# Performance work log

Hardware: AMD Instinct MI355X
Metric: run time of the kernel (lower is better)

The kernel has to match this reference:

```python
import jax, jax.numpy as jnp
import numpy as np

IMG_B, IMG_H, IMG_W, IMG_C = 16, 512, 1024, 3

def _base_grid(B, H, W):
    # replicates the module's custom normalization: arange/dim * 2 - 1
    base_x = (jnp.arange(W, dtype=jnp.float32) / W) * 2.0 - 1.0   # [W]
    base_y = (jnp.arange(H, dtype=jnp.float32) / H) * 2.0 - 1.0   # [H]
    base = jnp.stack([jnp.broadcast_to(base_x[None, :], (H, W)),
                      jnp.broadcast_to(base_y[:, None], (H, W))], axis=-1)  # [H,W,2]
    return jnp.broadcast_to(base[None], (B, H, W, 2))

def _grid_sample_bilinear_zeros(im, grid):
    # im: [B,C,H,W], grid: [B,Ho,Wo,2] in [-1,1], align_corners=False, zeros padding
    B, C, H, W = im.shape
    gx, gy = grid[..., 0], grid[..., 1]
    ix = ((gx + 1.0) * W - 1.0) * 0.5
    iy = ((gy + 1.0) * H - 1.0) * 0.5
    x0 = jnp.floor(ix); y0 = jnp.floor(iy)
    wx1 = ix - x0; wx0 = 1.0 - wx1
    wy1 = iy - y0; wy0 = 1.0 - wy1
    x0i = x0.astype(jnp.int32); y0i = y0.astype(jnp.int32)
    b_idx = jnp.arange(B, dtype=jnp.int32)[:, None, None]

    def corner(xi, yi, w):
        valid = (xi >= 0) & (xi < W) & (yi >= 0) & (yi < H)
        xc = jnp.clip(xi, 0, W - 1); yc = jnp.clip(yi, 0, H - 1)
        # advanced indexing -> [B,Ho,Wo,C]
        v = im[b_idx, :, yc, xc]
        return v * (w * valid.astype(im.dtype))[..., None]

    out = (corner(x0i,     y0i,     wx0 * wy0) +
           corner(x0i + 1, y0i,     wx1 * wy0) +
           corner(x0i,     y0i + 1, wx0 * wy1) +
           corner(x0i + 1, y0i + 1, wx1 * wy1))           # [B,Ho,Wo,C]
    return jnp.transpose(out, (0, 3, 1, 2))                # [B,C,Ho,Wo]

def setup_inputs() -> dict:
    key = jax.random.key(0)
    k1, k2, k3 = jax.random.split(key, 3)
    pred_flow = jax.random.normal(k1, (IMG_B, IMG_H, IMG_W, 2), dtype=jnp.float32) * 8.0
    im1_origin = jax.random.uniform(k2, (IMG_B, IMG_C, IMG_H, IMG_W), dtype=jnp.float32)
    im2_origin = jax.random.uniform(k3, (IMG_B, IMG_C, IMG_H, IMG_W), dtype=jnp.float32)
    return {"pred_flow": pred_flow, "im1_origin": im1_origin, "im2_origin": im2_origin}

def reference(pred_flow, im1_origin, im2_origin):
    B, H, W, _ = pred_flow.shape
    scale = jnp.array([W, H], dtype=pred_flow.dtype)
    grid = pred_flow / scale + _base_grid(B, H, W)
    im1_warp = _grid_sample_bilinear_zeros(im1_origin, grid)
    loss = jnp.sum(jnp.abs(im2_origin - im1_warp)) / (W * H)
    return loss
```

## Files before the change

### kernel.cpp

```cpp
#include <hip/hip_runtime.h>
#include <hip/hip_fp16.h>

namespace {

constexpr int B = 16, C = 3, H = 512, W = 1024;
constexpr int HW = H * W;
constexpr int SLABW = 256, SLABH = 64;
constexpr int XH  = 16;
constexpr int SWD = SLABW + 2 * XH;
constexpr int PAIRS = SWD / 2;
constexpr int PADP = 147;
constexpr int RING = 32;
constexpr int RA = 11;
constexpr int RB = 16;
constexpr int RPS = 4;
constexpr int BLOCK = 1024;
constexpr int TX = W / SLABW;
constexpr int TY = H / SLABH;
constexpr int GRID = B * TX * TY;
constexpr int PF_ROWS = RA + RB + 1;
constexpr int STG_P = C * RPS * PAIRS;
constexpr int CHS = RING * PADP;

constexpr float INV_W = 1.0f / 1024.0f;
constexpr float INV_H = 1.0f / 512.0f;

__device__ __forceinline__ float2 ld2g(const float* p) {
    struct __attribute__((packed, aligned(4))) F2 { float a, b; };
    const F2 v = *reinterpret_cast<const F2*>(p);
    return make_float2(v.a, v.b);
}

__device__ __forceinline__ uint32_t packh2(float a, float b) {
    return (uint32_t)__half_as_ushort(__float2half_rn(a))
         | ((uint32_t)__half_as_ushort(__float2half_rn(b)) << 16);
}
__device__ __forceinline__ float2 unpackh2(uint32_t u) {
    const __half2 h = __builtin_bit_cast(__half2, u);
    return make_float2(__low2float(h), __high2float(h));
}
__device__ __forceinline__ uint32_t alignsel(uint32_t hi, uint32_t lo, int sh) {
    return (uint32_t)(((((uint64_t)hi) << 32) | (uint64_t)lo) >> sh);
}

__global__ __launch_bounds__(BLOCK, 8) void flow_loss_partial(
    const float* __restrict__ flow,
    const float* __restrict__ im1,
    const float* __restrict__ im2,
    float* __restrict__ partials)
{
    __shared__ uint32_t sm32[C * CHS];
    __shared__ float red[BLOCK / 64];

    const int tid = threadIdx.x;
    const int bid = blockIdx.x;
    const int b   = bid >> 5;
    const int tt  = bid & 31;
    const int tyi = tt >> 2;
    const int txi = tt & 3;
    const int xbase  = txi * SLABW;
    const int yStart = tyi * SLABH;
    const int xb0    = xbase - XH;

    const float* __restrict__ im1b = im1 + b * C * HW;
    const float* __restrict__ im2b = im2 + b * C * HW;
    const float* __restrict__ flb  = flow + 2 * (b * HW);

    for (int e = tid; e < PF_ROWS * C * PAIRS; e += BLOCK) {
        const int q  = e % PAIRS;
        const int rc = e / PAIRS;
        const int c  = rc / PF_ROWS;
        const int ri = rc - c * PF_ROWS;
        const int row = yStart - RA + ri;
        if (row >= 0) {
            const int g0 = min(max(xb0 + 2 * q, 0), W - 1);
            const int g1 = min(max(xb0 + 2 * q + 1, 0), W - 1);
            const float a = im1b[c * HW + row * W + g0];
            const float d = im1b[c * HW + row * W + g1];
            sm32[c * CHS + (row & (RING - 1)) * PADP + q] = packh2(a, d);
        }
    }

    int  stSr[2], stG0[2], stG1[2], stL[2];
    const bool stOK1 = (tid < STG_P - BLOCK);
#pragma unroll
    for (int k = 0; k < 2; ++k) {
        const int e  = (k == 0) ? tid : (stOK1 ? BLOCK + tid : 0);
        const int q  = e % PAIRS;
        const int rc = e / PAIRS;
        const int c  = rc >> 2;
        stSr[k] = rc & 3;
        const int g0 = min(max(xb0 + 2 * q, 0), W - 1);
        const int g1 = min(max(xb0 + 2 * q + 1, 0), W - 1);
        stG0[k] = c * HW + g0;
        stG1[k] = c * HW + g1;
        stL[k]  = c * CHS + q;
    }

    auto issue = [&](int r0, int (&sIdx)[2], uint32_t (&sVal)[2]) {
#pragma unroll
        for (int k = 0; k < 2; ++k) {
            const int srow = r0 + stSr[k];
            int idx = -1; uint32_t v = 0;
            const bool act = (k == 0 || stOK1) & (srow < H);
            if (act) {
                const float a = im1b[stG0[k] + (srow << 10)];
                const float d = im1b[stG1[k] + (srow << 10)];
                v   = packh2(a, d);
                idx = stL[k] + (srow & (RING - 1)) * PADP;
            }
            sIdx[k] = idx; sVal[k] = v;
        }
    };

    int sIA[2]; uint32_t sVA[2];
    issue(yStart + RB + 1, sIA, sVA);

    const int colp = tid & (SLABW - 1);
    const int prow = tid >> 8;
    const int x = xbase + colp;
    const float base_x = (float)x * (2.0f * INV_W) - 1.0f;

    __syncthreads();

    float acc = 0.0f;

#pragma unroll 1
    for (int ys = yStart; ys < yStart + SLABH; ys += RPS) {
        int sIB[2]; uint32_t sVB[2];
        issue(ys + RB + 1 + RPS, sIB, sVB);

        const int y = ys + prow;
        const int zoff = y * W + x;
        const float2 f = *reinterpret_cast<const float2*>(flb + 2 * zoff);
        const float z0 = im2b[zoff];
        const float z1 = im2b[HW + zoff];
        const float z2 = im2b[2 * HW + zoff];

        const float base_y = (float)y * (2.0f * INV_H) - 1.0f;
        const float gx = __builtin_fmaf(f.x, INV_W, base_x);
        const float gy = __builtin_fmaf(f.y, INV_H, base_y);
        const float ixf = __builtin_fmaf(gx + 1.0f, 512.0f, -0.5f);
        const float iyf = __builtin_fmaf(gy + 1.0f, 256.0f, -0.5f);

        const float x0f = floorf(ixf), y0f = floorf(iyf);
        const float wx1 = ixf - x0f, wx0 = 1.0f - wx1;
        const float wy1 = iyf - y0f, wy0 = 1.0f - wy1;
        const int x0 = (int)x0f, y0 = (int)y0f;
        const int y1 = y0 + 1;
        const bool vx0 = (x0 >= 0) & (x0 < W);
        const bool vx1 = (x0 >= -1) & (x0 < W - 1);
        const bool vy0 = (y0 >= 0) & (y0 < H);
        const bool vy1 = (y1 >= 0) & (y1 < H);
        const bool s0 = (x0 >= W - 1), s1 = (x0 >= 0);

        const float px0 = wx0 * (float)vx0;
        const float px1 = wx1 * (float)vx1;
        const float u0 = (s0 ? 0.0f : px0) + (s1 ? 0.0f : px1);
        const float u1 = (s0 ? px0 : 0.0f) + (s1 ? px1 : 0.0f);
        const float mT = wy0 * (float)vy0;
        const float mB = wy1 * (float)vy1;
        const float aT0 = mT * u0, aT1 = mT * u1;
        const float aB0 = mB * u0, aB1 = mB * u1;

        const int xL  = min(max(x0, 0), W - 2);
        const int y0c = min(max(y0, 0), H - 1);
        const int y1c = min(max(y1, 0), H - 1);

        const int jj = xL - xbase + XH;
        const bool inR = (y0c >= ys - RA) & (y1c <= ys + RB) &
                         ((unsigned)jj <= (unsigned)(SWD - 2));

        float wp0, wp1, wp2;
        __builtin_amdgcn_s_setprio(1);
        if (inR) {
            const int q  = jj >> 1;
            const int sh = (jj & 1) << 4;
            const int aT = (y0c & (RING - 1)) * PADP + q;
            const int aB = (y1c & (RING - 1)) * PADP + q;
            const uint32_t dT0a = sm32[aT],           dT0b = sm32[aT + 1];
            const uint32_t dB0a = sm32[aB],           dB0b = sm32[aB + 1];
            const uint32_t dT1a = sm32[aT + CHS],     dT1b = sm32[aT + CHS + 1];
            const uint32_t dB1a = sm32[aB + CHS],     dB1b = sm32[aB + CHS + 1];
            const uint32_t dT2a = sm32[aT + 2 * CHS], dT2b = sm32[aT + 2 * CHS + 1];
            const uint32_t dB2a = sm32[aB + 2 * CHS], dB2b = sm32[aB + 2 * CHS + 1];
            const float2 t0 = unpackh2(alignsel(dT0b, dT0a, sh));
            const float2 b0 = unpackh2(alignsel(dB0b, dB0a, sh));
            const float2 t1 = unpackh2(alignsel(dT1b, dT1a, sh));
            const float2 b1 = unpackh2(alignsel(dB1b, dB1a, sh));
            const float2 t2 = unpackh2(alignsel(dT2b, dT2a, sh));
            const float2 b2 = unpackh2(alignsel(dB2b, dB2a, sh));
            wp0 = ((aT0 * t0.x + aT1 * t0.y) + aB0 * b0.x) + aB1 * b0.y;
            wp1 = ((aT0 * t1.x + aT1 * t1.y) + aB0 * b1.x) + aB1 * b1.y;
            wp2 = ((aT0 * t2.x + aT1 * t2.y) + aB0 * b2.x) + aB1 * b2.y;
        } else {
            const int oT = y0c * W + xL, oB = y1c * W + xL;
            const float2 ta = ld2g(im1b + oT),            ba = ld2g(im1b + oB);
            const float2 tb = ld2g(im1b + HW + oT),       bb = ld2g(im1b + HW + oB);
            const float2 tc = ld2g(im1b + 2 * HW + oT),   bc = ld2g(im1b + 2 * HW + oB);
            wp0 = ((aT0 * ta.x + aT1 * ta.y) + aB0 * ba.x) + aB1 * ba.y;
            wp1 = ((aT0 * tb.x + aT1 * tb.y) + aB0 * bb.x) + aB1 * bb.y;
            wp2 = ((aT0 * tc.x + aT1 * tc.y) + aB0 * bc.x) + aB1 * bc.y;
        }
        acc += fabsf(z0 - wp0) + fabsf(z1 - wp1) + fabsf(z2 - wp2);
        __builtin_amdgcn_s_setprio(0);

#pragma unroll
        for (int k = 0; k < 2; ++k)
            if (sIA[k] >= 0) sm32[sIA[k]] = sVA[k];
        __syncthreads();

#pragma unroll
        for (int k = 0; k < 2; ++k) { sIA[k] = sIB[k]; sVA[k] = sVB[k]; }
    }

#pragma unroll
    for (int o = 32; o > 0; o >>= 1)
        acc += __shfl_down(acc, o, 64);
    const int lane = tid & 63;
    const int wid  = tid >> 6;
    if (lane == 0) red[wid] = acc;
    __syncthreads();
    if (tid == 0) {
        float s = 0.0f;
#pragma unroll
        for (int wv = 0; wv < BLOCK / 64; ++wv) s += red[wv];
        partials[bid] = s;
    }
}

__global__ __launch_bounds__(256) void flow_loss_reduce(
    const float* __restrict__ partials, float* __restrict__ out)
{
    __shared__ double lds[256];
    double acc = 0.0;
    for (int i = threadIdx.x; i < GRID; i += 256) acc += (double)partials[i];
    lds[threadIdx.x] = acc;
    __syncthreads();
    for (int o = 128; o > 0; o >>= 1) {
        if (threadIdx.x < o) lds[threadIdx.x] += lds[threadIdx.x + o];
        __syncthreads();
    }
    if (threadIdx.x == 0) out[0] = (float)(lds[0] / (double)(W * H));
}

}

extern "C" void kernel_launch(void* const* d_in, const int* in_sizes, int n_in,
                              void* d_out, int out_size, void* d_ws, size_t ws_size,
                              hipStream_t stream) {
    const float* flow = (const float*)d_in[0];
    const float* im1  = (const float*)d_in[1];
    const float* im2  = (const float*)d_in[2];
    float* out = (float*)d_out;
    float* partials = (float*)d_ws;

    flow_loss_partial<<<GRID, BLOCK, 0, stream>>>(flow, im1, im2, partials);
    flow_loss_reduce<<<1, 256, 0, stream>>>(partials, out);
}
```

Before: 58.40 us.

## Process two rows per thread per step and halve ring-buffer barriers

Each thread now handles two output rows per iteration (RPS doubled to 8), so the number of __syncthreads and staging rounds per slab is halved and each thread has more independent loads in flight. The staging now issues 4 pairs per thread with packed sub-row indices and reuses a single address base for the second element. The ring window margins (RA/RB) shrink to fit the larger step inside the 32-row ring, which sends more samples with large vertical flow to the slower global fallback path. When either of the two rows misses the window, both take the global path, which adds divergence.

After: 225.9 us. +286.9%, slower.

```diff
diff --git a/kernel.cpp b/kernel.cpp
--- a/kernel.cpp
+++ b/kernel.cpp
@@ -11,15 +11,16 @@
 constexpr int PAIRS = SWD / 2;
 constexpr int PADP = 147;
 constexpr int RING = 32;
-constexpr int RA = 11;
-constexpr int RB = 16;
-constexpr int RPS = 4;
+constexpr int RA = 9;
+constexpr int RB = 14;
+constexpr int RPS = 8;
 constexpr int BLOCK = 1024;
 constexpr int TX = W / SLABW;
 constexpr int TY = H / SLABH;
 constexpr int GRID = B * TX * TY;
 constexpr int PF_ROWS = RA + RB + 1;
 constexpr int STG_P = C * RPS * PAIRS;
+constexpr int NK = 4;
 constexpr int CHS = RING * PADP;
 
 constexpr float INV_W = 1.0f / 1024.0f;
@@ -81,31 +82,35 @@
         }
     }
 
-    int  stSr[2], stG0[2], stG1[2], stL[2];
-    const bool stOK1 = (tid < STG_P - BLOCK);
-#pragma unroll
-    for (int k = 0; k < 2; ++k) {
-        const int e  = (k == 0) ? tid : (stOK1 ? BLOCK + tid : 0);
+    int stG0[NK], stL[NK];
+    uint32_t stSrPack = 0, stPiBits = 0;
+    const bool stOK3 = (tid < STG_P - 3 * BLOCK);
+#pragma unroll
+    for (int k = 0; k < NK; ++k) {
+        const int e  = (k < 3) ? (k * BLOCK + tid) : (stOK3 ? 3 * BLOCK + tid : 0);
         const int q  = e % PAIRS;
         const int rc = e / PAIRS;
-        const int c  = rc >> 2;
-        stSr[k] = rc & 3;
-        const int g0 = min(max(xb0 + 2 * q, 0), W - 1);
-        const int g1 = min(max(xb0 + 2 * q + 1, 0), W - 1);
-        stG0[k] = c * HW + g0;
-        stG1[k] = c * HW + g1;
+        const int c  = rc >> 3;
+        const int sr = rc & 7;
+        stSrPack |= (uint32_t)sr << (8 * k);
+        const int p  = xb0 + 2 * q;
+        const bool pi = (p >= 0) & (p <= W - 2);
+        stPiBits |= (uint32_t)pi << k;
+        stG0[k] = c * HW + (pi ? p : min(max(p, 0), W - 1));
         stL[k]  = c * CHS + q;
     }
 
-    auto issue = [&](int r0, int (&sIdx)[2], uint32_t (&sVal)[2]) {
-#pragma unroll
-        for (int k = 0; k < 2; ++k) {
-            const int srow = r0 + stSr[k];
+    auto issue = [&](int r0, int (&sIdx)[NK], uint32_t (&sVal)[NK]) {
+#pragma unroll
+        for (int k = 0; k < NK; ++k) {
+            const int sr   = (int)((stSrPack >> (8 * k)) & 0xffu);
+            const int srow = r0 + sr;
             int idx = -1; uint32_t v = 0;
-            const bool act = (k == 0 || stOK1) & (srow < H);
+            const bool act = (k < 3 || stOK3) & (srow < H);
             if (act) {
-                const float a = im1b[stG0[k] + (srow << 10)];
-                const float d = im1b[stG1[k] + (srow << 10)];
+                const int g0 = stG0[k] + (srow << 10);
+                const float a = im1b[g0];
+                const float d = im1b[g0 + (int)((stPiBits >> k) & 1u)];
                 v   = packh2(a, d);
                 idx = stL[k] + (srow & (RING - 1)) * PADP;
             }
@@ -113,7 +118,7 @@
         }
     };
 
-    int sIA[2]; uint32_t sVA[2];
+    int sIA[NK]; uint32_t sVA[NK];
     issue(yStart + RB + 1, sIA, sVA);
 
     const int colp = tid & (SLABW - 1);
@@ -125,24 +130,14 @@
 
     float acc = 0.0f;
 
-#pragma unroll 1
-    for (int ys = yStart; ys < yStart + SLABH; ys += RPS) {
-        int sIB[2]; uint32_t sVB[2];
-        issue(ys + RB + 1 + RPS, sIB, sVB);
-
-        const int y = ys + prow;
-        const int zoff = y * W + x;
-        const float2 f = *reinterpret_cast<const float2*>(flb + 2 * zoff);
-        const float z0 = im2b[zoff];
-        const float z1 = im2b[HW + zoff];
-        const float z2 = im2b[2 * HW + zoff];
-
+    auto geom = [&](int y, float2 f, int ys_,
+                    float& aT0, float& aT1, float& aB0, float& aB1,
+                    int& xL, int& y0c, int& y1c, int& jj) -> bool {
         const float base_y = (float)y * (2.0f * INV_H) - 1.0f;
         const float gx = __builtin_fmaf(f.x, INV_W, base_x);
         const float gy = __builtin_fmaf(f.y, INV_H, base_y);
         const float ixf = __builtin_fmaf(gx + 1.0f, 512.0f, -0.5f);
         const float iyf = __builtin_fmaf(gy + 1.0f, 256.0f, -0.5f);
-
         const float x0f = floorf(ixf), y0f = floorf(iyf);
         const float wx1 = ixf - x0f, wx0 = 1.0f - wx1;
         const float wy1 = iyf - y0f, wy0 = 1.0f - wy1;
@@ -153,65 +148,89 @@
         const bool vy0 = (y0 >= 0) & (y0 < H);
         const bool vy1 = (y1 >= 0) & (y1 < H);
         const bool s0 = (x0 >= W - 1), s1 = (x0 >= 0);
-
         const float px0 = wx0 * (float)vx0;
         const float px1 = wx1 * (float)vx1;
         const float u0 = (s0 ? 0.0f : px0) + (s1 ? 0.0f : px1);
         const float u1 = (s0 ? px0 : 0.0f) + (s1 ? px1 : 0.0f);
         const float mT = wy0 * (float)vy0;
         const float mB = wy1 * (float)vy1;
-        const float aT0 = mT * u0, aT1 = mT * u1;
-        const float aB0 = mB * u0, aB1 = mB * u1;
-
-        const int xL  = min(max(x0, 0), W - 2);
-        const int y0c = min(max(y0, 0), H - 1);
-        const int y1c = min(max(y1, 0), H - 1);
-
-        const int jj = xL - xbase + XH;
-        const bool inR = (y0c >= ys - RA) & (y1c <= ys + RB) &
-                         ((unsigned)jj <= (unsigned)(SWD - 2));
-
-        float wp0, wp1, wp2;
+        aT0 = mT * u0; aT1 = mT * u1; aB0 = mB * u0; aB1 = mB * u1;
+        xL  = min(max(x0, 0), W - 2);
+        y0c = min(max(y0, 0), H - 1);
+        y1c = min(max(y1, 0), H - 1);
+        jj  = xL - xbase + XH;
+        return (y0c >= ys_ - RA) & (y1c <= ys_ + RB) &
+               ((unsigned)jj <= (unsigned)(SWD - 2));
+    };
+
+    auto gpath = [&](float aT0, float aT1, float aB0, float aB1,
+                     int xL, int y0c, int y1c, float z0, float z1, float z2) -> float {
+        const int oT = y0c * W + xL, oB = y1c * W + xL;
+        const float2 ta = ld2g(im1b + oT),            ba = ld2g(im1b + oB);
+        const float2 tb = ld2g(im1b + HW + oT),       bb = ld2g(im1b + HW + oB);
+        const float2 tc = ld2g(im1b + 2 * HW + oT),   bc = ld2g(im1b + 2 * HW + oB);
+        const float wp0 = ((aT0 * ta.x + aT1 * ta.y) + aB0 * ba.x) + aB1 * ba.y;
+        const float wp1 = ((aT0 * tb.x + aT1 * tb.y) + aB0 * bb.x) + aB1 * bb.y;
+        const float wp2 = ((aT0 * tc.x + aT1 * tc.y) + aB0 * bc.x) + aB1 * bc.y;
+        return fabsf(z0 - wp0) + fabsf(z1 - wp1) + fabsf(z2 - wp2);
+    };
+
+#pragma unroll 1
+    for (int ys = yStart; ys < yStart + SLABH; ys += RPS) {
+        int sIB[NK]; uint32_t sVB[NK];
+        issue(ys + RB + 1 + RPS, sIB, sVB);
+
+        const int yA = ys + prow;
+        const int zoffA = yA * W + x;
+        const int zoffB = zoffA + 4 * W;
+        const float2 fA = *reinterpret_cast<const float2*>(flb + 2 * zoffA);
+        const float2 fB = *reinterpret_cast<const float2*>(flb + 2 * zoffB);
+        const float zA0 = im2b[zoffA], zA1 = im2b[HW + zoffA], zA2 = im2b[2 * HW + zoffA];
+        const float zB0 = im2b[zoffB], zB1 = im2b[HW + zoffB], zB2 = im2b[2 * HW + zoffB];
+
+        float aT0A, aT1A, aB0A, aB1A, aT0B, aT1B, aB0B, aB1B;
+        int   xLA, y0cA, y1cA, jjA, xLB, y0cB, y1cB, jjB;
+        const bool inRA = geom(yA,     fA, ys, aT0A, aT1A, aB0A, aB1A, xLA, y0cA, y1cA, jjA);
+        const bool inRB = geom(yA + 4, fB, ys, aT0B, aT1B, aB0B, aB1B, xLB, y0cB, y1cB, jjB);
+
         __builtin_amdgcn_s_setprio(1);
-        if (inR) {
-            const int q  = jj >> 1;
-            const int sh = (jj & 1) << 4;
-            const int aT = (y0c & (RING - 1)) * PADP + q;
-            const int aB = (y1c & (RING - 1)) * PADP + q;
-            const uint32_t dT0a = sm32[aT],           dT0b = sm32[aT + 1];
-            const uint32_t dB0a = sm32[aB],           dB0b = sm32[aB + 1];
-            const uint32_t dT1a = sm32[aT + CHS],     dT1b = sm32[aT + CHS + 1];
-            const uint32_t dB1a = sm32[aB + CHS],     dB1b = sm32[aB + CHS + 1];
-            const uint32_t dT2a = sm32[aT + 2 * CHS], dT2b = sm32[aT + 2 * CHS + 1];
-            const uint32_t dB2a = sm32[aB + 2 * CHS], dB2b = sm32[aB + 2 * CHS + 1];
-            const float2 t0 = unpackh2(alignsel(dT0b, dT0a, sh));
-            const float2 b0 = unpackh2(alignsel(dB0b, dB0a, sh));
-            const float2 t1 = unpackh2(alignsel(dT1b, dT1a, sh));
-            const float2 b1 = unpackh2(alignsel(dB1b, dB1a, sh));
-            const float2 t2 = unpackh2(alignsel(dT2b, dT2a, sh));
-            const float2 b2 = unpackh2(alignsel(dB2b, dB2a, sh));
-            wp0 = ((aT0 * t0.x + aT1 * t0.y) + aB0 * b0.x) + aB1 * b0.y;
-            wp1 = ((aT0 * t1.x + aT1 * t1.y) + aB0 * b1.x) + aB1 * b1.y;
-            wp2 = ((aT0 * t2.x + aT1 * t2.y) + aB0 * b2.x) + aB1 * b2.y;
+        if (inRA & inRB) {
+            const int qA = jjA >> 1, shA = (jjA & 1) << 4;
+            const int lTA = (y0cA & (RING - 1)) * PADP + qA;
+            const int lBA = (y1cA & (RING - 1)) * PADP + qA;
+            const int qB = jjB >> 1, shB = (jjB & 1) << 4;
+            const int lTB = (y0cB & (RING - 1)) * PADP + qB;
+            const int lBB = (y1cB & (RING - 1)) * PADP + qB;
+#pragma unroll
+            for (int c = 0; c < C; ++c) {
+                const int o = c * CHS;
+                const uint32_t tAa = sm32[o + lTA], tAb = sm32[o + lTA + 1];
+                const uint32_t bAa = sm32[o + lBA], bAb = sm32[o + lBA + 1];
+                const uint32_t tBa = sm32[o + lTB], tBb = sm32[o + lTB + 1];
+                const uint32_t bBa = sm32[o + lBB], bBb = sm32[o + lBB + 1];
+                const float2 tA = unpackh2(alignsel(tAb, tAa, shA));
+                const float2 bA = unpackh2(alignsel(bAb, bAa, shA));
+                const float2 tB = unpackh2(alignsel(tBb, tBa, shB));
+                const float2 bB = unpackh2(alignsel(bBb, bBa, shB));
+                const float wpA = ((aT0A * tA.x + aT1A * tA.y) + aB0A * bA.x) + aB1A * bA.y;
+                const float wpB = ((aT0B * tB.x + aT1B * tB.y) + aB0B * bB.x) + aB1B * bB.y;
+                const float zA = (c == 0) ? zA0 : ((c == 1) ? zA1 : zA2);
+                const float zB = (c == 0) ? zB0 : ((c == 1) ? zB1 : zB2);
+                acc += fabsf(zA - wpA) + fabsf(zB - wpB);
+            }
         } else {
-            const int oT = y0c * W + xL, oB = y1c * W + xL;
-            const float2 ta = ld2g(im1b + oT),            ba = ld2g(im1b + oB);
-            const float2 tb = ld2g(im1b + HW + oT),       bb = ld2g(im1b + HW + oB);
-            const float2 tc = ld2g(im1b + 2 * HW + oT),   bc = ld2g(im1b + 2 * HW + oB);
-            wp0 = ((aT0 * ta.x + aT1 * ta.y) + aB0 * ba.x) + aB1 * ba.y;
-            wp1 = ((aT0 * tb.x + aT1 * tb.y) + aB0 * bb.x) + aB1 * bb.y;
-            wp2 = ((aT0 * tc.x + aT1 * tc.y) + aB0 * bc.x) + aB1 * bc.y;
+            acc += gpath(aT0A, aT1A, aB0A, aB1A, xLA, y0cA, y1cA, zA0, zA1, zA2);
+            acc += gpath(aT0B, aT1B, aB0B, aB1B, xLB, y0cB, y1cB, zB0, zB1, zB2);
         }
-        acc += fabsf(z0 - wp0) + fabsf(z1 - wp1) + fabsf(z2 - wp2);
         __builtin_amdgcn_s_setprio(0);
 
 #pragma unroll
-        for (int k = 0; k < 2; ++k)
+        for (int k = 0; k < NK; ++k)
             if (sIA[k] >= 0) sm32[sIA[k]] = sVA[k];
         __syncthreads();
 
 #pragma unroll
-        for (int k = 0; k < 2; ++k) { sIA[k] = sIB[k]; sVA[k] = sVB[k]; }
+        for (int k = 0; k < NK; ++k) { sIA[k] = sIB[k]; sVA[k] = sVB[k]; }
     }
 
 #pragma unroll
```
